# Kernel tuning notes

Measured on AMD Instinct MI355X. Metric: run time of the kernel, lower is better.

Reference implementation:

```python
import jax, jax.numpy as jnp
import numpy as np

# Directional rectangle cumulative max: max over the axis-aligned rectangle
# between each pixel and one image corner.

def _rectmax(x, rev_h, rev_w):
    y = jax.lax.cummax(x, axis=2, reverse=rev_h)
    return jax.lax.cummax(y, axis=3, reverse=rev_w)


def _guided_pool(xq, gq, rev_h, rev_w):
    # Guided landmark pool: each pixel takes max of itself and the directional
    # cumulative max restricted to guide==1 positions. With guide == ones this
    # reduces to the plain directional rectangle cummax (the un-guided pool).
    neg = jnp.finfo(xq.dtype).min
    masked = jnp.where(gq > 0, xq, neg)
    return jnp.maximum(xq, _rectmax(masked, rev_h, rev_w))

# (rev_h, rev_w) for TopLeft, TopRight, BottomLeft, BottomRight pools
_DIRS = [(True, True), (True, False), (False, True), (False, False)]


def setup_inputs() -> dict:
    key = jax.random.key(0)
    k1, k2, k3 = jax.random.split(key, 3)
    B, C, H, W = 16, 256, 64, 64
    Cout, K = 256, 3
    x = jax.random.normal(k1, (B, C, H, W), jnp.float32)
    weight = jax.random.normal(k2, (Cout, C, K, K), jnp.float32) * 0.02
    bias = jax.random.normal(k3, (Cout,), jnp.float32) * 0.02
    return {"x": x, "weight": weight, "bias": bias}


def reference(x, weight, bias):
    B, C, H, W = x.shape
    Q = C // 4
    # Original torch code squares x IN PLACE via chunk() views before pooling.
    xsq = x * x
    # Per-quadrant channel energy and its global (row, col) argmax -> one-hot guide.
    energy = xsq.reshape(B, 4, Q, H, W).sum(axis=2)            # [B,4,H,W]
    idx = jnp.argmax(energy.reshape(B, 4, H * W), axis=-1)     # [B,4]
    onehot = (jnp.arange(H * W) == idx[..., None]).astype(x.dtype)
    guide = jnp.broadcast_to(onehot.reshape(B, 4, 1, H, W), (B, 4, Q, H, W)).reshape(B, C, H, W)
    # Four directional guided pools, one per channel quadrant, then conv.
    xs = jnp.split(xsq, 4, axis=1)
    gs = jnp.split(guide, 4, axis=1)
    pooled = jnp.concatenate(
        [_guided_pool(xs[i], gs[i], *_DIRS[i]) for i in range(4)], axis=1)
    out = jax.lax.conv_general_dilated(
        pooled, weight, window_strides=(1, 1), padding='SAME',
        dimension_numbers=('NCHW', 'OIHW', 'NCHW'))
    return out + bias[None, :, None, None]
```

## Files before the change

### kernel.cpp

```cpp
#include <hip/hip_runtime.h>
#include <cstddef>

#define B_   16
#define C_   256
#define HW_  4096

typedef __attribute__((ext_vector_type(8)))  short bf16x8;
typedef __attribute__((ext_vector_type(16))) float f32x16;

static __device__ __forceinline__ unsigned short f2bf(float f) {
    unsigned int u = __float_as_uint(f);
    u += 0x7fffu + ((u >> 16) & 1u);
    return (unsigned short)(u >> 16);
}

__global__ __launch_bounds__(256) void fused_energy(const float* __restrict__ x,
                                                    unsigned short* __restrict__ xsqN,
                                                    float* __restrict__ pval,
                                                    int* __restrict__ pidx) {
    int blk = blockIdx.x;
    int b = blk >> 6, h = blk & 63;
    int tid = threadIdx.x;
    int w = tid & 63, layer = tid >> 6;
    __shared__ float earr[4][4][64];
    __shared__ unsigned short tile[64][264];
    float e0 = 0.f, e1 = 0.f, e2 = 0.f, e3 = 0.f;
    const float* xb = x + (size_t)b * C_ * HW_ + h * 64 + w;
#pragma unroll
    for (int i = 0; i < 8; ++i) {
        int c0 = (i * 4 + layer) * 8;
        union { unsigned short us[8]; int4 v; } u;
        float es = 0.f;
#pragma unroll
        for (int k = 0; k < 8; ++k) {
            float v = xb[(size_t)(c0 + k) * HW_];
            float s = v * v;
            es += s;
            u.us[k] = f2bf(s);
        }
        *(int4*)&tile[w][c0] = u.v;
        if ((i >> 1) == 0) e0 += es;
        else if ((i >> 1) == 1) e1 += es;
        else if ((i >> 1) == 2) e2 += es;
        else e3 += es;
    }
    earr[layer][0][w] = e0; earr[layer][1][w] = e1;
    earr[layer][2][w] = e2; earr[layer][3][w] = e3;
    __syncthreads();
    size_t base = (size_t)(b * 64 + h) * 64 * 256;
#pragma unroll
    for (int it = 0; it < 8; ++it) {
        int row  = it * 8 + (tid >> 5);
        int col8 = (tid & 31) * 8;
        *(int4*)(xsqN + base + (size_t)row * 256 + col8) = *(int4*)&tile[row][col8];
    }
    int q = tid >> 6;
    float ev = earr[0][q][w] + earr[1][q][w] + earr[2][q][w] + earr[3][q][w];
    int ix = h * 64 + w;
#pragma unroll
    for (int off = 32; off; off >>= 1) {
        float ov = __shfl_down(ev, off);
        int   oi = __shfl_down(ix, off);
        if (ov > ev || (ov == ev && oi < ix)) { ev = ov; ix = oi; }
    }
    if ((tid & 63) == 0) {
        pval[(b * 64 + h) * 4 + q] = ev;
        pidx[(b * 64 + h) * 4 + q] = ix;
    }
}

__global__ __launch_bounds__(64) void energy_final(const float* __restrict__ pval,
                                                   const int* __restrict__ pidx,
                                                   int* __restrict__ lm) {
    int bq = blockIdx.x;
    int b = bq >> 2, q = bq & 3;
    int h = threadIdx.x;
    float ev = pval[(b * 64 + h) * 4 + q];
    int   ix = pidx[(b * 64 + h) * 4 + q];
#pragma unroll
    for (int off = 32; off; off >>= 1) {
        float ov = __shfl_down(ev, off);
        int   oi = __shfl_down(ix, off);
        if (ov > ev || (ov == ev && oi < ix)) { ev = ov; ix = oi; }
    }
    if (h == 0) lm[bq] = ix;
}

__global__ __launch_bounds__(256) void lval_kernel(const unsigned short* __restrict__ xsqN,
                                                   const int* __restrict__ lm,
                                                   unsigned short* __restrict__ Lval) {
    int t = blockIdx.x * 256 + threadIdx.x;
    int b = t >> 8, c = t & 255, q = c >> 6;
    int l = lm[b * 4 + q];
    Lval[t] = xsqN[((size_t)((b * 64 + (l >> 6)) * 64 + (l & 63))) * 256 + c];
}

__global__ __launch_bounds__(64) void wt_pack(const float* __restrict__ w,
                                              unsigned short* __restrict__ wa) {
    int blk  = blockIdx.x;
    int lane = threadIdx.x;
    int cog = blk & 7;
    int s   = (blk >> 3) & 1;
    int cib = (blk >> 4) & 7;
    int j   = blk >> 7;
    int co  = cog * 32 + (lane & 31);
    int k0  = cib * 32 + s * 16 + (lane >> 5) * 8;
    union { unsigned short us[8]; int4 v; } u;
#pragma unroll
    for (int jj = 0; jj < 8; ++jj) {
        int ci = k0 + jj;
        u.us[jj] = f2bf(w[(size_t)(co * 256 + ci) * 9 + j]);
    }
    *(int4*)(wa + ((size_t)blk * 64 + lane) * 8) = u.v;
}

__global__ __launch_bounds__(512, 2) void conv_mfma(const unsigned short* __restrict__ xsqN,
                                                    const unsigned short* __restrict__ wa,
                                                    const float* __restrict__ bias,
                                                    const int* __restrict__ lm,
                                                    const unsigned short* __restrict__ Lval,
                                                    float* __restrict__ out) {
    int pt = blockIdx.x;
    int b  = pt >> 4;
    int h0 = (pt & 15) * 4;
    int tid  = threadIdx.x;
    int lane = tid & 63;
    int wv   = tid >> 6;
    int wy = wv >> 2, wx = wv & 3;
    int l31 = lane & 31, qh = lane >> 5;

    __shared__ unsigned short Bs[2][6 * 66 * 40];
    __shared__ unsigned short As[2][8192];

    f32x16 acc[4][2];
#pragma unroll
    for (int mt = 0; mt < 4; ++mt)
#pragma unroll
        for (int nt = 0; nt < 2; ++nt)
#pragma unroll
            for (int r = 0; r < 16; ++r) acc[mt][nt][r] = 0.f;

    int4 sv[4];
    int4 av0, av1;

    {
#pragma unroll
        for (int t2 = 0; t2 < 4; ++t2) {
            int idx = tid + t2 * 512;
            int4 v = {0, 0, 0, 0};
            if (idx < 1584) {
                int pr = idx / 264; int rem = idx - pr * 264;
                int pc = rem >> 2;  int part = rem & 3;
                int grow = h0 - 1 + pr, gcol = pc - 1;
                if ((unsigned)grow < 64u && (unsigned)gcol < 64u)
                    v = *(const int4*)(xsqN + (((size_t)(b * 64 + grow) * 64 + gcol) * 256 + part * 8));
            }
            sv[t2] = v;
        }
        int l = lm[b * 4 + 0];
        int hm = l >> 6, wm = l & 63;
#pragma unroll
        for (int t2 = 0; t2 < 4; ++t2) {
            int idx = tid + t2 * 512;
            if (idx < 1584) {
                int pr = idx / 264; int rem = idx - pr * 264;
                int pc = rem >> 2;  int part = rem & 3;
                int grow = h0 - 1 + pr, gcol = pc - 1;
                union { int4 v; unsigned short us[8]; } u; u.v = sv[t2];
                bool inb = ((unsigned)grow < 64u) && ((unsigned)gcol < 64u);
                if (inb && grow <= hm && gcol <= wm) {
                    union { int4 v; unsigned short us[8]; } Lu;
                    Lu.v = *(const int4*)(Lval + b * 256 + part * 8);
#pragma unroll
                    for (int k = 0; k < 8; ++k)
                        if (Lu.us[k] > u.us[k]) u.us[k] = Lu.us[k];
                }
                *(int4*)(&Bs[0][(pr * 66 + pc) * 40 + part * 8]) = u.v;
            }
        }
        const unsigned short* src = wa + tid * 16;
        av0 = *(const int4*)src;
        av1 = *(const int4*)(src + 8);
        *(int4*)(&As[0][tid * 16])     = av0;
        *(int4*)(&As[0][tid * 16 + 8]) = av1;
    }
    __syncthreads();

    for (int cib = 0; cib < 8; ++cib) {
        for (int j = 0; j < 9; ++j) {
            int p = cib * 9 + j;
            bool hasNext = (p < 71);
            if (hasNext) {
                int jn = j + 1, cibn = cib;
                if (jn == 9) { jn = 0; cibn = cib + 1; }
                const unsigned short* src = wa + ((size_t)(jn * 8 + cibn) << 13) + tid * 16;
                av0 = *(const int4*)src;
                av1 = *(const int4*)(src + 8);
            }
            if (j == 0 && cib < 7) {
                int nc = cib + 1;
#pragma unroll
                for (int t2 = 0; t2 < 4; ++t2) {
                    int idx = tid + t2 * 512;
                    int4 v = {0, 0, 0, 0};
                    if (idx < 1584) {
                        int pr = idx / 264; int rem = idx - pr * 264;
                        int pc = rem >> 2;  int part = rem & 3;
                        int grow = h0 - 1 + pr, gcol = pc - 1;
                        if ((unsigned)grow < 64u && (unsigned)gcol < 64u)
                            v = *(const int4*)(xsqN + (((size_t)(b * 64 + grow) * 64 + gcol) * 256 + nc * 32 + part * 8));
                    }
                    sv[t2] = v;
                }
            }

            {
                const unsigned short* Ab = &As[p & 1][0];
                const unsigned short* Bb = &Bs[cib & 1][0];
                int dh = j / 3 - 1, dw = j % 3 - 1;
                int r  = wx + dh + 1;
                int w0 = l31 + dw + 1;
#pragma unroll
                for (int s = 0; s < 2; ++s) {
                    const bf16x8* ap = (const bf16x8*)(Ab + (((s * 8 + wy * 4) * 64 + lane) << 3));
                    bf16x8 a0 = ap[0];
                    bf16x8 a1 = ap[64];
                    bf16x8 a2 = ap[128];
                    bf16x8 a3 = ap[192];
                    bf16x8 b0 = *(const bf16x8*)(Bb + (r * 66 + w0) * 40 + s * 16 + qh * 8);
                    bf16x8 b1 = *(const bf16x8*)(Bb + (r * 66 + w0 + 32) * 40 + s * 16 + qh * 8);
                    acc[0][0] = __builtin_amdgcn_mfma_f32_32x32x16_bf16(a0, b0, acc[0][0], 0, 0, 0);
                    acc[0][1] = __builtin_amdgcn_mfma_f32_32x32x16_bf16(a0, b1, acc[0][1], 0, 0, 0);
                    acc[1][0] = __builtin_amdgcn_mfma_f32_32x32x16_bf16(a1, b0, acc[1][0], 0, 0, 0);
                    acc[1][1] = __builtin_amdgcn_mfma_f32_32x32x16_bf16(a1, b1, acc[1][1], 0, 0, 0);
                    acc[2][0] = __builtin_amdgcn_mfma_f32_32x32x16_bf16(a2, b0, acc[2][0], 0, 0, 0);
                    acc[2][1] = __builtin_amdgcn_mfma_f32_32x32x16_bf16(a2, b1, acc[2][1], 0, 0, 0);
                    acc[3][0] = __builtin_amdgcn_mfma_f32_32x32x16_bf16(a3, b0, acc[3][0], 0, 0, 0);
                    acc[3][1] = __builtin_amdgcn_mfma_f32_32x32x16_bf16(a3, b1, acc[3][1], 0, 0, 0);
                }
            }

            if (j == 8 && cib < 7) {
                int nc = cib + 1;
                int l = lm[b * 4 + (nc >> 1)];
                int hm = l >> 6, wm = l & 63;
                bool qhle = (nc >> 1) < 2;
                bool qwle = ((nc >> 1) & 1) == 0;
                unsigned short* Bw = &Bs[(cib + 1) & 1][0];
#pragma unroll
                for (int t2 = 0; t2 < 4; ++t2) {
                    int idx = tid + t2 * 512;
                    if (idx < 1584) {
                        int pr = idx / 264; int rem = idx - pr * 264;
                        int pc = rem >> 2;  int part = rem & 3;
                        int grow = h0 - 1 + pr, gcol = pc - 1;
                        union { int4 v; unsigned short us[8]; } u; u.v = sv[t2];
                        bool inb = ((unsigned)grow < 64u) && ((unsigned)gcol < 64u);
                        bool hok = qhle ? (grow <= hm) : (grow >= hm);
                        bool wok = qwle ? (gcol <= wm) : (gcol >= wm);
                        if (inb && hok && wok) {
                            union { int4 v; unsigned short us[8]; } Lu;
                            Lu.v = *(const int4*)(Lval + b * 256 + nc * 32 + part * 8);
#pragma unroll
                            for (int k = 0; k < 8; ++k)
                                if (Lu.us[k] > u.us[k]) u.us[k] = Lu.us[k];
                        }
                        *(int4*)(&Bw[(pr * 66 + pc) * 40 + part * 8]) = u.v;
                    }
                }
            }
            if (hasNext) {
                unsigned short* dst = &As[(p + 1) & 1][tid * 16];
                *(int4*)dst       = av0;
                *(int4*)(dst + 8) = av1;
            }
            __syncthreads();
        }
    }

    int h = h0 + wx;
#pragma unroll
    for (int mt = 0; mt < 4; ++mt) {
#pragma unroll
        for (int nt = 0; nt < 2; ++nt) {
#pragma unroll
            for (int r = 0; r < 16; ++r) {
                int row = (r & 3) + 8 * (r >> 2) + 4 * qh;
                int co  = wy * 128 + mt * 32 + row;
                int w   = nt * 32 + l31;
                out[(((size_t)(b * 256 + co)) * 64 + h) * 64 + w] = acc[mt][nt][r] + bias[co];
            }
        }
    }
}

extern "C" void kernel_launch(void* const* d_in, const int* in_sizes, int n_in,
                              void* d_out, int out_size, void* d_ws, size_t ws_size,
                              hipStream_t stream) {
    const float* x      = (const float*)d_in[0];
    const float* weight = (const float*)d_in[1];
    const float* bias   = (const float*)d_in[2];
    float* out = (float*)d_out;

    char* ws = (char*)d_ws;
    int*            lmp  = (int*)ws;
    float*          pval = (float*)(ws + 256);
    int*            pidx = (int*)(ws + 256 + 16384);
    unsigned short* Lval = (unsigned short*)(ws + 256 + 32768);
    unsigned short* Wa   = (unsigned short*)(ws + 49152);
    unsigned short* xsqN = (unsigned short*)(ws + 49152 + 1179648);

    hipLaunchKernelGGL(fused_energy, dim3(1024), dim3(256), 0, stream, x, xsqN, pval, pidx);
    hipLaunchKernelGGL(energy_final, dim3(64), dim3(64), 0, stream, pval, pidx, lmp);
    hipLaunchKernelGGL(lval_kernel, dim3(16), dim3(256), 0, stream, xsqN, lmp, Lval);
    hipLaunchKernelGGL(wt_pack, dim3(1152), dim3(64), 0, stream, weight, Wa);
    hipLaunchKernelGGL(conv_mfma, dim3(256), dim3(512), 0, stream, xsqN, Wa, bias, lmp, Lval, out);
}
```

Measured before the change: 199.4 us.

## Load conv weights directly from global into registers, sync once per channel block

Removes the shared-memory staging of weight fragments. Each wave now reads its bf16 A operands straight from global memory (L2/L1 cached) inside the 9-tap loop, which drops the per-tap __syncthreads to one barrier per channel block. It also wraps the MFMA groups in s_setprio to favour the matrix issue. The trade is more global or L1 traffic for weights, plus exposed load latency that is no longer overlapped by the explicit prefetch, in exchange for less LDS use and far fewer barriers.

```diff
diff --git a/kernel.cpp b/kernel.cpp
--- a/kernel.cpp
+++ b/kernel.cpp
@@ -130,7 +130,6 @@
     int l31 = lane & 31, qh = lane >> 5;
 
     __shared__ unsigned short Bs[2][6 * 66 * 40];
-    __shared__ unsigned short As[2][8192];
 
     f32x16 acc[4][2];
 #pragma unroll
@@ -141,7 +140,6 @@
             for (int r = 0; r < 16; ++r) acc[mt][nt][r] = 0.f;
 
     int4 sv[4];
-    int4 av0, av1;
 
     {
 #pragma unroll
@@ -178,104 +176,103 @@
                 *(int4*)(&Bs[0][(pr * 66 + pc) * 40 + part * 8]) = u.v;
             }
         }
-        const unsigned short* src = wa + tid * 16;
-        av0 = *(const int4*)src;
-        av1 = *(const int4*)(src + 8);
-        *(int4*)(&As[0][tid * 16])     = av0;
-        *(int4*)(&As[0][tid * 16 + 8]) = av1;
     }
     __syncthreads();
 
+    const bf16x8* Abase = (const bf16x8*)wa + (wy << 8) + lane;
+
     for (int cib = 0; cib < 8; ++cib) {
+        if (cib < 7) {
+            int nc = cib + 1;
+#pragma unroll
+            for (int t2 = 0; t2 < 4; ++t2) {
+                int idx = tid + t2 * 512;
+                int4 v = {0, 0, 0, 0};
+                if (idx < 1584) {
+                    int pr = idx / 264; int rem = idx - pr * 264;
+                    int pc = rem >> 2;  int part = rem & 3;
+                    int grow = h0 - 1 + pr, gcol = pc - 1;
+                    if ((unsigned)grow < 64u && (unsigned)gcol < 64u)
+                        v = *(const int4*)(xsqN + (((size_t)(b * 64 + grow) * 64 + gcol) * 256 + nc * 32 + part * 8));
+                }
+                sv[t2] = v;
+            }
+        }
+
+        const bf16x8* Ac = Abase + ((size_t)cib << 10);
+        const unsigned short* Bb = &Bs[cib & 1][0];
+
         for (int j = 0; j < 9; ++j) {
-            int p = cib * 9 + j;
-            bool hasNext = (p < 71);
-            if (hasNext) {
-                int jn = j + 1, cibn = cib;
-                if (jn == 9) { jn = 0; cibn = cib + 1; }
-                const unsigned short* src = wa + ((size_t)(jn * 8 + cibn) << 13) + tid * 16;
-                av0 = *(const int4*)src;
-                av1 = *(const int4*)(src + 8);
-            }
-            if (j == 0 && cib < 7) {
-                int nc = cib + 1;
-#pragma unroll
-                for (int t2 = 0; t2 < 4; ++t2) {
-                    int idx = tid + t2 * 512;
-                    int4 v = {0, 0, 0, 0};
-                    if (idx < 1584) {
-                        int pr = idx / 264; int rem = idx - pr * 264;
-                        int pc = rem >> 2;  int part = rem & 3;
-                        int grow = h0 - 1 + pr, gcol = pc - 1;
-                        if ((unsigned)grow < 64u && (unsigned)gcol < 64u)
-                            v = *(const int4*)(xsqN + (((size_t)(b * 64 + grow) * 64 + gcol) * 256 + nc * 32 + part * 8));
+            const bf16x8* Ag = Ac + (size_t)j * 8192;
+            bf16x8 a00 = Ag[0];
+            bf16x8 a01 = Ag[64];
+            bf16x8 a02 = Ag[128];
+            bf16x8 a03 = Ag[192];
+            bf16x8 a10 = Ag[512];
+            bf16x8 a11 = Ag[576];
+            bf16x8 a12 = Ag[640];
+            bf16x8 a13 = Ag[704];
+
+            int j3 = j / 3;
+            int dh = j3 - 1, dw = (j - j3 * 3) - 1;
+            int r  = wx + dh + 1;
+            int w0 = l31 + dw + 1;
+            const unsigned short* Bp = Bb + (r * 66 + w0) * 40 + qh * 8;
+            bf16x8 b00 = *(const bf16x8*)(Bp);
+            bf16x8 b01 = *(const bf16x8*)(Bp + 1280);
+            bf16x8 b10 = *(const bf16x8*)(Bp + 16);
+            bf16x8 b11 = *(const bf16x8*)(Bp + 1296);
+
+            __builtin_amdgcn_s_setprio(1);
+            acc[0][0] = __builtin_amdgcn_mfma_f32_32x32x16_bf16(a00, b00, acc[0][0], 0, 0, 0);
+            acc[0][1] = __builtin_amdgcn_mfma_f32_32x32x16_bf16(a00, b01, acc[0][1], 0, 0, 0);
+            acc[1][0] = __builtin_amdgcn_mfma_f32_32x32x16_bf16(a01, b00, acc[1][0], 0, 0, 0);
+            acc[1][1] = __builtin_amdgcn_mfma_f32_32x32x16_bf16(a01, b01, acc[1][1], 0, 0, 0);
+            acc[2][0] = __builtin_amdgcn_mfma_f32_32x32x16_bf16(a02, b00, acc[2][0], 0, 0, 0);
+            acc[2][1] = __builtin_amdgcn_mfma_f32_32x32x16_bf16(a02, b01, acc[2][1], 0, 0, 0);
+            acc[3][0] = __builtin_amdgcn_mfma_f32_32x32x16_bf16(a03, b00, acc[3][0], 0, 0, 0);
+            acc[3][1] = __builtin_amdgcn_mfma_f32_32x32x16_bf16(a03, b01, acc[3][1], 0, 0, 0);
+            acc[0][0] = __builtin_amdgcn_mfma_f32_32x32x16_bf16(a10, b10, acc[0][0], 0, 0, 0);
+            acc[0][1] = __builtin_amdgcn_mfma_f32_32x32x16_bf16(a10, b11, acc[0][1], 0, 0, 0);
+            acc[1][0] = __builtin_amdgcn_mfma_f32_32x32x16_bf16(a11, b10, acc[1][0], 0, 0, 0);
+            acc[1][1] = __builtin_amdgcn_mfma_f32_32x32x16_bf16(a11, b11, acc[1][1], 0, 0, 0);
+            acc[2][0] = __builtin_amdgcn_mfma_f32_32x32x16_bf16(a12, b10, acc[2][0], 0, 0, 0);
+            acc[2][1] = __builtin_amdgcn_mfma_f32_32x32x16_bf16(a12, b11, acc[2][1], 0, 0, 0);
+            acc[3][0] = __builtin_amdgcn_mfma_f32_32x32x16_bf16(a13, b10, acc[3][0], 0, 0, 0);
+            acc[3][1] = __builtin_amdgcn_mfma_f32_32x32x16_bf16(a13, b11, acc[3][1], 0, 0, 0);
+            __builtin_amdgcn_s_setprio(0);
+        }
+
+        if (cib < 7) {
+            int nc = cib + 1;
+            int l = lm[b * 4 + (nc >> 1)];
+            int hm = l >> 6, wm = l & 63;
+            bool qhle = (nc >> 1) < 2;
+            bool qwle = ((nc >> 1) & 1) == 0;
+            unsigned short* Bw = &Bs[(cib + 1) & 1][0];
+#pragma unroll
+            for (int t2 = 0; t2 < 4; ++t2) {
+                int idx = tid + t2 * 512;
+                if (idx < 1584) {
+                    int pr = idx / 264; int rem = idx - pr * 264;
+                    int pc = rem >> 2;  int part = rem & 3;
+                    int grow = h0 - 1 + pr, gcol = pc - 1;
+                    union { int4 v; unsigned short us[8]; } u; u.v = sv[t2];
+                    bool inb = ((unsigned)grow < 64u) && ((unsigned)gcol < 64u);
+                    bool hok = qhle ? (grow <= hm) : (grow >= hm);
+                    bool wok = qwle ? (gcol <= wm) : (gcol >= wm);
+                    if (inb && hok && wok) {
+                        union { int4 v; unsigned short us[8]; } Lu;
+                        Lu.v = *(const int4*)(Lval + b * 256 + nc * 32 + part * 8);
+#pragma unroll
+                        for (int k = 0; k < 8; ++k)
+                            if (Lu.us[k] > u.us[k]) u.us[k] = Lu.us[k];
                     }
-                    sv[t2] = v;
+                    *(int4*)(&Bw[(pr * 66 + pc) * 40 + part * 8]) = u.v;
                 }
             }
-
-            {
-                const unsigned short* Ab = &As[p & 1][0];
-                const unsigned short* Bb = &Bs[cib & 1][0];
-                int dh = j / 3 - 1, dw = j % 3 - 1;
-                int r  = wx + dh + 1;
-                int w0 = l31 + dw + 1;
-#pragma unroll
-                for (int s = 0; s < 2; ++s) {
-                    const bf16x8* ap = (const bf16x8*)(Ab + (((s * 8 + wy * 4) * 64 + lane) << 3));
-                    bf16x8 a0 = ap[0];
-                    bf16x8 a1 = ap[64];
-                    bf16x8 a2 = ap[128];
-                    bf16x8 a3 = ap[192];
-                    bf16x8 b0 = *(const bf16x8*)(Bb + (r * 66 + w0) * 40 + s * 16 + qh * 8);
-                    bf16x8 b1 = *(const bf16x8*)(Bb + (r * 66 + w0 + 32) * 40 + s * 16 + qh * 8);
-                    acc[0][0] = __builtin_amdgcn_mfma_f32_32x32x16_bf16(a0, b0, acc[0][0], 0, 0, 0);
-                    acc[0][1] = __builtin_amdgcn_mfma_f32_32x32x16_bf16(a0, b1, acc[0][1], 0, 0, 0);
-                    acc[1][0] = __builtin_amdgcn_mfma_f32_32x32x16_bf16(a1, b0, acc[1][0], 0, 0, 0);
-                    acc[1][1] = __builtin_amdgcn_mfma_f32_32x32x16_bf16(a1, b1, acc[1][1], 0, 0, 0);
-                    acc[2][0] = __builtin_amdgcn_mfma_f32_32x32x16_bf16(a2, b0, acc[2][0], 0, 0, 0);
-                    acc[2][1] = __builtin_amdgcn_mfma_f32_32x32x16_bf16(a2, b1, acc[2][1], 0, 0, 0);
-                    acc[3][0] = __builtin_amdgcn_mfma_f32_32x32x16_bf16(a3, b0, acc[3][0], 0, 0, 0);
-                    acc[3][1] = __builtin_amdgcn_mfma_f32_32x32x16_bf16(a3, b1, acc[3][1], 0, 0, 0);
-                }
-            }
-
-            if (j == 8 && cib < 7) {
-                int nc = cib + 1;
-                int l = lm[b * 4 + (nc >> 1)];
-                int hm = l >> 6, wm = l & 63;
-                bool qhle = (nc >> 1) < 2;
-                bool qwle = ((nc >> 1) & 1) == 0;
-                unsigned short* Bw = &Bs[(cib + 1) & 1][0];
-#pragma unroll
-                for (int t2 = 0; t2 < 4; ++t2) {
-                    int idx = tid + t2 * 512;
-                    if (idx < 1584) {
-                        int pr = idx / 264; int rem = idx - pr * 264;
-                        int pc = rem >> 2;  int part = rem & 3;
-                        int grow = h0 - 1 + pr, gcol = pc - 1;
-                        union { int4 v; unsigned short us[8]; } u; u.v = sv[t2];
-                        bool inb = ((unsigned)grow < 64u) && ((unsigned)gcol < 64u);
-                        bool hok = qhle ? (grow <= hm) : (grow >= hm);
-                        bool wok = qwle ? (gcol <= wm) : (gcol >= wm);
-                        if (inb && hok && wok) {
-                            union { int4 v; unsigned short us[8]; } Lu;
-                            Lu.v = *(const int4*)(Lval + b * 256 + nc * 32 + part * 8);
-#pragma unroll
-                            for (int k = 0; k < 8; ++k)
-                                if (Lu.us[k] > u.us[k]) u.us[k] = Lu.us[k];
-                        }
-                        *(int4*)(&Bw[(pr * 66 + pc) * 40 + part * 8]) = u.v;
-                    }
-                }
-            }
-            if (hasNext) {
-                unsigned short* dst = &As[(p + 1) & 1][tid * 16];
-                *(int4*)dst       = av0;
-                *(int4*)(dst + 8) = av1;
-            }
-            __syncthreads();
-        }
+        }
+        __syncthreads();
     }
 
     int h = h0 + wx;
```

Result: no change. 201.6 us (+1.1%).

## Vectorize energy loads, fuse landmark gather, coalesce weight packing via LDS

Applied to the files above, without the earlier changes.

The energy kernel now loads x with float4 along width, with each thread covering 4 pixels by 4 channels, and reduces quadrant energies across lanes with xor shuffles. The separate landmark-value kernel is folded into energy_final, which removes one launch. Weight packing now stages contiguous float4 reads of weights in LDS and transposes them there, replacing strided scalar global reads. The goal is fewer launches and more coalesced memory traffic in the prep stages, at the cost of more complex indexing and more LDS writes.

```diff
diff --git a/kernel.cpp b/kernel.cpp
--- a/kernel.cpp
+++ b/kernel.cpp
@@ -21,32 +21,58 @@
     int blk = blockIdx.x;
     int b = blk >> 6, h = blk & 63;
     int tid = threadIdx.x;
-    int w = tid & 63, layer = tid >> 6;
+    int tl  = tid >> 4;
+    int w4  = (tid & 15) << 2;
+    int wv  = tid >> 6;
     __shared__ float earr[4][4][64];
     __shared__ unsigned short tile[64][264];
-    float e0 = 0.f, e1 = 0.f, e2 = 0.f, e3 = 0.f;
-    const float* xb = x + (size_t)b * C_ * HW_ + h * 64 + w;
-#pragma unroll
-    for (int i = 0; i < 8; ++i) {
-        int c0 = (i * 4 + layer) * 8;
-        union { unsigned short us[8]; int4 v; } u;
-        float es = 0.f;
-#pragma unroll
-        for (int k = 0; k < 8; ++k) {
-            float v = xb[(size_t)(c0 + k) * HW_];
-            float s = v * v;
-            es += s;
-            u.us[k] = f2bf(s);
-        }
-        *(int4*)&tile[w][c0] = u.v;
-        if ((i >> 1) == 0) e0 += es;
-        else if ((i >> 1) == 1) e1 += es;
-        else if ((i >> 1) == 2) e2 += es;
-        else e3 += es;
-    }
-    earr[layer][0][w] = e0; earr[layer][1][w] = e1;
-    earr[layer][2][w] = e2; earr[layer][3][w] = e3;
+    const float* xb = x + (size_t)b * C_ * HW_ + h * 64 + w4;
+
+    float e[4][4];
+#pragma unroll
+    for (int q = 0; q < 4; ++q)
+#pragma unroll
+        for (int ww = 0; ww < 4; ++ww) e[q][ww] = 0.f;
+
+#pragma unroll
+    for (int i = 0; i < 4; ++i) {
+        int c4 = tl * 4 + 64 * i;
+        float sq[4][4];
+#pragma unroll
+        for (int k = 0; k < 4; ++k) {
+            float4 v = *(const float4*)(xb + (size_t)(c4 + k) * HW_);
+            sq[k][0] = v.x * v.x; sq[k][1] = v.y * v.y;
+            sq[k][2] = v.z * v.z; sq[k][3] = v.w * v.w;
+            e[i][0] += sq[k][0]; e[i][1] += sq[k][1];
+            e[i][2] += sq[k][2]; e[i][3] += sq[k][3];
+        }
+#pragma unroll
+        for (int ww = 0; ww < 4; ++ww) {
+            uint2 p;
+            p.x = (unsigned)f2bf(sq[0][ww]) | ((unsigned)f2bf(sq[1][ww]) << 16);
+            p.y = (unsigned)f2bf(sq[2][ww]) | ((unsigned)f2bf(sq[3][ww]) << 16);
+            *(uint2*)(&tile[w4 + ww][c4]) = p;
+        }
+    }
+
+#pragma unroll
+    for (int q = 0; q < 4; ++q)
+#pragma unroll
+        for (int ww = 0; ww < 4; ++ww) {
+            float v = e[q][ww];
+            v += __shfl_xor(v, 16);
+            v += __shfl_xor(v, 32);
+            e[q][ww] = v;
+        }
+    if ((tid & 48) == 0) {
+#pragma unroll
+        for (int q = 0; q < 4; ++q) {
+            float4 v; v.x = e[q][0]; v.y = e[q][1]; v.z = e[q][2]; v.w = e[q][3];
+            *(float4*)&earr[wv][q][w4] = v;
+        }
+    }
     __syncthreads();
+
     size_t base = (size_t)(b * 64 + h) * 64 * 256;
 #pragma unroll
     for (int it = 0; it < 8; ++it) {
@@ -54,7 +80,9 @@
         int col8 = (tid & 31) * 8;
         *(int4*)(xsqN + base + (size_t)row * 256 + col8) = *(int4*)&tile[row][col8];
     }
+
     int q = tid >> 6;
+    int w = tid & 63;
     float ev = earr[0][q][w] + earr[1][q][w] + earr[2][q][w] + earr[3][q][w];
     int ix = h * 64 + w;
 #pragma unroll
@@ -71,47 +99,59 @@
 
 __global__ __launch_bounds__(64) void energy_final(const float* __restrict__ pval,
                                                    const int* __restrict__ pidx,
-                                                   int* __restrict__ lm) {
+                                                   int* __restrict__ lm,
+                                                   const unsigned short* __restrict__ xsqN,
+                                                   unsigned short* __restrict__ Lval) {
     int bq = blockIdx.x;
     int b = bq >> 2, q = bq & 3;
-    int h = threadIdx.x;
-    float ev = pval[(b * 64 + h) * 4 + q];
-    int   ix = pidx[(b * 64 + h) * 4 + q];
+    int t = threadIdx.x;
+    float ev = pval[(b * 64 + t) * 4 + q];
+    int   ix = pidx[(b * 64 + t) * 4 + q];
 #pragma unroll
     for (int off = 32; off; off >>= 1) {
         float ov = __shfl_down(ev, off);
         int   oi = __shfl_down(ix, off);
         if (ov > ev || (ov == ev && oi < ix)) { ev = ov; ix = oi; }
     }
-    if (h == 0) lm[bq] = ix;
-}
-
-__global__ __launch_bounds__(256) void lval_kernel(const unsigned short* __restrict__ xsqN,
-                                                   const int* __restrict__ lm,
-                                                   unsigned short* __restrict__ Lval) {
-    int t = blockIdx.x * 256 + threadIdx.x;
-    int b = t >> 8, c = t & 255, q = c >> 6;
-    int l = lm[b * 4 + q];
-    Lval[t] = xsqN[((size_t)((b * 64 + (l >> 6)) * 64 + (l & 63))) * 256 + c];
-}
-
-__global__ __launch_bounds__(64) void wt_pack(const float* __restrict__ w,
-                                              unsigned short* __restrict__ wa) {
-    int blk  = blockIdx.x;
-    int lane = threadIdx.x;
-    int cog = blk & 7;
-    int s   = (blk >> 3) & 1;
-    int cib = (blk >> 4) & 7;
-    int j   = blk >> 7;
-    int co  = cog * 32 + (lane & 31);
-    int k0  = cib * 32 + s * 16 + (lane >> 5) * 8;
-    union { unsigned short us[8]; int4 v; } u;
-#pragma unroll
-    for (int jj = 0; jj < 8; ++jj) {
-        int ci = k0 + jj;
-        u.us[jj] = f2bf(w[(size_t)(co * 256 + ci) * 9 + j]);
-    }
-    *(int4*)(wa + ((size_t)blk * 64 + lane) * 8) = u.v;
+    int ix0 = __shfl(ix, 0);
+    if (t == 0) lm[bq] = ix0;
+    Lval[b * 256 + q * 64 + t] =
+        xsqN[((size_t)((b * 64 + (ix0 >> 6)) * 64 + (ix0 & 63))) * 256 + q * 64 + t];
+}
+
+__global__ __launch_bounds__(256) void wt_pack(const float* __restrict__ w,
+                                               unsigned short* __restrict__ wa) {
+    int blk = blockIdx.x;
+    int cog = blk >> 3, cib = blk & 7;
+    int tid = threadIdx.x;
+    __shared__ unsigned short wlds[32][292];
+    {
+        int co_l = tid >> 3;
+        int seg  = tid & 7;
+        const float* src = w + ((size_t)((cog * 32 + co_l) * 256 + cib * 32)) * 9 + seg * 36;
+#pragma unroll
+        for (int f4 = 0; f4 < 9; ++f4) {
+            float4 v = *(const float4*)(src + f4 * 4);
+            uint2 p;
+            p.x = (unsigned)f2bf(v.x) | ((unsigned)f2bf(v.y) << 16);
+            p.y = (unsigned)f2bf(v.z) | ((unsigned)f2bf(v.w) << 16);
+            *(uint2*)(&wlds[co_l][seg * 36 + f4 * 4]) = p;
+        }
+    }
+    __syncthreads();
+    for (int idx = tid; idx < 1152; idx += 256) {
+        int lane = idx & 63;
+        int s    = (idx >> 6) & 1;
+        int j    = idx >> 7;
+        int co_l = lane & 31;
+        int k0   = s * 16 + (lane >> 5) * 8;
+        union { unsigned short us[8]; int4 v; } u;
+#pragma unroll
+        for (int jj = 0; jj < 8; ++jj)
+            u.us[jj] = wlds[co_l][(k0 + jj) * 9 + j];
+        int ob = j * 128 + cib * 16 + s * 8 + cog;
+        *(int4*)(wa + ((size_t)ob * 64 + lane) * 8) = u.v;
+    }
 }
 
 __global__ __launch_bounds__(512, 2) void conv_mfma(const unsigned short* __restrict__ xsqN,
@@ -311,8 +351,7 @@
     unsigned short* xsqN = (unsigned short*)(ws + 49152 + 1179648);
 
     hipLaunchKernelGGL(fused_energy, dim3(1024), dim3(256), 0, stream, x, xsqN, pval, pidx);
-    hipLaunchKernelGGL(energy_final, dim3(64), dim3(64), 0, stream, pval, pidx, lmp);
-    hipLaunchKernelGGL(lval_kernel, dim3(16), dim3(256), 0, stream, xsqN, lmp, Lval);
-    hipLaunchKernelGGL(wt_pack, dim3(1152), dim3(64), 0, stream, weight, Wa);
+    hipLaunchKernelGGL(energy_final, dim3(64), dim3(64), 0, stream, pval, pidx, lmp, xsqN, Lval);
+    hipLaunchKernelGGL(wt_pack, dim3(64), dim3(256), 0, stream, weight, Wa);
     hipLaunchKernelGGL(conv_mfma, dim3(256), dim3(512), 0, stream, xsqN, Wa, bias, lmp, Lval, out);
 }
```

Result: no change. 196.2 us (-1.6%).
